# Kernel optimization log

Measured on AMD Instinct MI355X. Metric: run time of the kernel, lower is better.

Reference implementation:

```python
import jax, jax.numpy as jnp
import numpy as np

NUM_TOKENS = 1024  # codebook size (n_embed)
CODE_DIM = 256     # embedding_dim
BETA = 0.25


def setup_inputs() -> dict:
    key = jax.random.key(0)
    k1, k2 = jax.random.split(key)
    z = jax.random.normal(k1, (64, 512, CODE_DIM), dtype=jnp.float32)
    weight = jax.random.normal(k2, (NUM_TOKENS, CODE_DIM), dtype=jnp.float32)
    return {"z": z, "weight": weight}


def reference(z, weight):
    # z: [B, T, D]; weight: [K, D]
    z_flat = z.reshape(-1, CODE_DIM)                       # [N, D]
    # squared euclidean distances: ||z||^2 + ||w||^2 - 2 z.w
    d = (jnp.sum(z_flat ** 2, axis=1, keepdims=True)
         + jnp.sum(weight ** 2, axis=1)
         - 2.0 * jnp.matmul(z_flat, weight.T))             # [N, K]
    min_encoding_indices = jnp.argmin(d, axis=1)           # [N]
    z_q = weight[min_encoding_indices].reshape(z.shape)    # gather

    # perplexity from mean one-hot usage (avoid materializing one-hot via bincount)
    counts = jnp.bincount(min_encoding_indices, length=NUM_TOKENS)
    e_mean = counts.astype(z.dtype) / z_flat.shape[0]
    perplexity = jnp.exp(-jnp.sum(e_mean * jnp.log(e_mean + 1e-10)))

    # commitment loss (codebook is EMA-updated, so z_q is detached)
    loss = BETA * jnp.mean((jax.lax.stop_gradient(z_q) - z) ** 2)
    # straight-through estimator
    z_q_st = z + jax.lax.stop_gradient(z_q - z)
    return (loss, z_q_st, min_encoding_indices, perplexity)
```

## Files before the change

kernel.cpp:

```cpp
#include <hip/hip_runtime.h>

#define N_TOKENS 32768
#define K_CODES  1024
#define DIM      256
#define BETA     0.25f

typedef unsigned long long u64;
typedef _Float16 half8 __attribute__((ext_vector_type(8)));
typedef float floatx4 __attribute__((ext_vector_type(4)));

__device__ __forceinline__ int gsw(int row, int g) {
    return g ^ ((row ^ (row >> 2)) & 3);
}

__global__ void init_kernel(const float* __restrict__ w, float* __restrict__ wn,
                            int* __restrict__ counts, u64* __restrict__ keys,
                            _Float16* __restrict__ whiG, _Float16* __restrict__ wloG) {
    int k = blockIdx.x;
    int lane = threadIdx.x;
    float4 v = *(const float4*)(w + (size_t)k * DIM + lane * 4);
    float vals[4] = {v.x, v.y, v.z, v.w};
    float s = 0.f;
    #pragma unroll
    for (int e = 0; e < 4; e++) {
        s += vals[e] * vals[e];
        _Float16 h = (_Float16)vals[e];
        whiG[k * DIM + lane * 4 + e] = h;
        wloG[k * DIM + lane * 4 + e] = (_Float16)(vals[e] - (float)h);
    }
    #pragma unroll
    for (int off = 32; off; off >>= 1) s += __shfl_down(s, off);
    if (lane == 0) { wn[k] = s; counts[k] = 0; }
    if (lane < 32) keys[k * 32 + lane] = ~0ull;
}

__global__ __launch_bounds__(256, 3) void argmin_kernel(
    const float* __restrict__ z, const _Float16* __restrict__ whiG,
    const _Float16* __restrict__ wloG, const float* __restrict__ wn,
    u64* __restrict__ keys)
{
    __shared__ _Float16 zhi[128 * 32], zlo[128 * 32];
    __shared__ _Float16 whi[128 * 32], wlo[128 * 32];

    const int tid  = threadIdx.x;
    const int lane = tid & 63;
    const int wid  = tid >> 6;
    const int wm   = wid >> 1;
    const int wq   = wid & 1;
    const int t_   = blockIdx.x & 255;
    const int q    = blockIdx.x >> 8;
    const int tok0  = t_ * 128;
    const int kbase = q * 128;

    const int n  = lane & 15;
    const int kg = lane >> 4;
    const int ga = kg ^ ((n ^ (n >> 2)) & 3);

    float wnv[4];
    #pragma unroll
    for (int j = 0; j < 4; j++)
        wnv[j] = wn[kbase + wq * 64 + j * 16 + n];

    floatx4 acc[4][4];
    #pragma unroll
    for (int i = 0; i < 4; i++)
        #pragma unroll
        for (int j = 0; j < 4; j++)
            acc[i][j] = (floatx4){0.f, 0.f, 0.f, 0.f};

    const int r0 = tid >> 2;
    const int g0 = tid & 3;

    for (int dt = 0; dt < 8; ++dt) {
        const int d0 = dt * 32;
        __syncthreads();

        #pragma unroll
        for (int s = 0; s < 2; s++) {
            int t = r0 + s * 64;
            const float* p = z + (size_t)(tok0 + t) * DIM + d0 + g0 * 8;
            float4 a = *(const float4*)p;
            float4 b = *(const float4*)(p + 4);
            float vals[8] = {a.x, a.y, a.z, a.w, b.x, b.y, b.z, b.w};
            half8 hv, lv;
            #pragma unroll
            for (int e = 0; e < 8; e++) {
                _Float16 h = (_Float16)vals[e];
                hv[e] = h;
                lv[e] = (_Float16)(vals[e] - (float)h);
            }
            int off = t * 32 + gsw(t, g0) * 8;
            *(half8*)&zhi[off] = hv;
            *(half8*)&zlo[off] = lv;
        }
        #pragma unroll
        for (int s = 0; s < 2; s++) {
            int t = r0 + s * 64;
            size_t goff = (size_t)(kbase + t) * DIM + d0 + g0 * 8;
            int off = t * 32 + gsw(t, g0) * 8;
            *(half8*)&whi[off] = *(const half8*)&whiG[goff];
            *(half8*)&wlo[off] = *(const half8*)&wloG[goff];
        }
        __syncthreads();

        half8 ah[4], al[4];
        #pragma unroll
        for (int i = 0; i < 4; i++) {
            int off = (wm * 64 + i * 16 + n) * 32 + ga * 8;
            ah[i] = *(const half8*)&zhi[off];
            al[i] = *(const half8*)&zlo[off];
        }
        #pragma unroll
        for (int j = 0; j < 4; j++) {
            int off = (wq * 64 + j * 16 + n) * 32 + ga * 8;
            half8 bh = *(const half8*)&whi[off];
            half8 bl = *(const half8*)&wlo[off];
            #pragma unroll
            for (int i = 0; i < 4; i++) {
                acc[i][j] = __builtin_amdgcn_mfma_f32_16x16x32_f16(ah[i], bh, acc[i][j], 0, 0, 0);
                acc[i][j] = __builtin_amdgcn_mfma_f32_16x16x32_f16(ah[i], bl, acc[i][j], 0, 0, 0);
                acc[i][j] = __builtin_amdgcn_mfma_f32_16x16x32_f16(al[i], bh, acc[i][j], 0, 0, 0);
            }
        }
    }

    #pragma unroll
    for (int i = 0; i < 4; i++) {
        #pragma unroll
        for (int r = 0; r < 4; r++) {
            float bv = 3.4e38f; int bi = 0;
            #pragma unroll
            for (int j = 0; j < 4; j++) {
                float dist = wnv[j] - 2.0f * acc[i][j][r];
                if (dist < bv) { bv = dist; bi = kbase + wq * 64 + j * 16 + n; }
            }
            unsigned uu = __float_as_uint(bv);
            unsigned ss = (uu & 0x80000000u) ? ~uu : (uu | 0x80000000u);
            u64 key = ((u64)ss << 32) | (unsigned)bi;
            #pragma unroll
            for (int m = 1; m < 16; m <<= 1) {
                u64 o = __shfl_xor(key, m);
                if (o < key) key = o;
            }
            if (n == 0) {
                int token = tok0 + wm * 64 + i * 16 + kg * 4 + r;
                atomicMin(&keys[token], key);
            }
        }
    }
}

__global__ void gather_loss_kernel(const float* __restrict__ z,
                                   const float* __restrict__ w,
                                   const u64* __restrict__ keys,
                                   float* __restrict__ zq_out,
                                   float* __restrict__ idxf,
                                   int* __restrict__ counts,
                                   float* __restrict__ partials)
{
    __shared__ float red[4];
    int tid = threadIdx.x;
    int lane = tid & 63;
    int wid = blockIdx.x * 4 + (tid >> 6);
    u64 k4[4];
    #pragma unroll
    for (int it = 0; it < 4; it++)
        k4[it] = keys[wid + it * 8192];
    float s = 0.0f;
    #pragma unroll
    for (int it = 0; it < 4; it++) {
        int tok = wid + it * 8192;
        int k = (int)(unsigned)(k4[it] & 0xFFFFFFFFull);
        float4 wv = *(const float4*)(w + (size_t)k * DIM + lane * 4);
        float4 zv = *(const float4*)(z + (size_t)tok * DIM + lane * 4);
        *(float4*)(zq_out + (size_t)tok * DIM + lane * 4) = wv;
        float dx = wv.x - zv.x, dy = wv.y - zv.y, dz = wv.z - zv.z, dw = wv.w - zv.w;
        s += dx * dx + dy * dy + dz * dz + dw * dw;
        if (lane == 0) {
            idxf[tok] = (float)k;
            atomicAdd(&counts[k], 1);
        }
    }
    #pragma unroll
    for (int off = 32; off; off >>= 1) s += __shfl_down(s, off);
    if (lane == 0) red[tid >> 6] = s;
    __syncthreads();
    if (tid == 0)
        partials[blockIdx.x] = red[0] + red[1] + red[2] + red[3];
}

__global__ void finalize_kernel(const int* __restrict__ counts,
                                const float* __restrict__ partials,
                                float* __restrict__ loss_out,
                                float* __restrict__ ppl_out)
{
    __shared__ float redE[16], redL[16];
    int tid = threadIdx.x;
    float e = (float)counts[tid] * (1.0f / (float)N_TOKENS);
    float t = -e * logf(e + 1e-10f);
    float p = partials[tid] + partials[tid + 1024];
    #pragma unroll
    for (int off = 32; off; off >>= 1) {
        t += __shfl_down(t, off);
        p += __shfl_down(p, off);
    }
    if ((tid & 63) == 0) { redE[tid >> 6] = t; redL[tid >> 6] = p; }
    __syncthreads();
    if (tid == 0) {
        float se = 0.0f, sl = 0.0f;
        #pragma unroll
        for (int i = 0; i < 16; i++) { se += redE[i]; sl += redL[i]; }
        *ppl_out = expf(se);
        *loss_out = BETA * sl / (float)((size_t)N_TOKENS * DIM);
    }
}

extern "C" void kernel_launch(void* const* d_in, const int* in_sizes, int n_in,
                              void* d_out, int out_size, void* d_ws, size_t ws_size,
                              hipStream_t stream) {
    const float* z = (const float*)d_in[0];
    const float* w = (const float*)d_in[1];
    float* out = (float*)d_out;

    float* loss_out = out;
    float* zq_out   = out + 1;
    float* idxf     = out + 1 + (size_t)N_TOKENS * DIM;
    float* ppl_out  = out + (out_size - 1);

    float* wn       = (float*)d_ws;
    int*   counts   = (int*)d_ws + 1024;
    float* partials = (float*)d_ws + 2048;
    u64*   keys     = (u64*)((char*)d_ws + 16384);
    _Float16* whiG  = (_Float16*)((char*)d_ws + 16384 + (size_t)N_TOKENS * 8);
    _Float16* wloG  = whiG + (size_t)K_CODES * DIM;

    init_kernel<<<K_CODES, 64, 0, stream>>>(w, wn, counts, keys, whiG, wloG);
    argmin_kernel<<<8 * 256, 256, 0, stream>>>(z, whiG, wloG, wn, keys);
    gather_loss_kernel<<<2048, 256, 0, stream>>>(z, w, keys, zq_out, idxf, counts, partials);
    finalize_kernel<<<1, 1024, 0, stream>>>(counts, partials, loss_out, ppl_out);
}
```

Measured before the change: 164.1 us.

## Pre-split z into packed fp16 hi/lo tiles and fuse finalize into gather

Adds a prep kernel that converts z once into fp16 hi/lo pairs stored in the exact swizzled shared-memory tile layout, using the output buffer as scratch. The weight is packed the same way, so the argmin kernel's inner loop becomes plain contiguous 16-byte copies with no fp32 loads or conversions. Before, each z tile was reconverted by all 8 codebook-quarter blocks. The finalize kernel is also folded into the gather kernel through a last-block atomic counter, which removes one launch. The cost is an extra full pass over z plus writing and rereading the packed copy.

```diff
diff --git a/kernel.cpp b/kernel.cpp
--- a/kernel.cpp
+++ b/kernel.cpp
@@ -7,6 +7,7 @@
 
 typedef unsigned long long u64;
 typedef _Float16 half8 __attribute__((ext_vector_type(8)));
+typedef _Float16 half4 __attribute__((ext_vector_type(4)));
 typedef float floatx4 __attribute__((ext_vector_type(4)));
 
 __device__ __forceinline__ int gsw(int row, int g) {
@@ -15,29 +16,65 @@
 
 __global__ void init_kernel(const float* __restrict__ w, float* __restrict__ wn,
                             int* __restrict__ counts, u64* __restrict__ keys,
-                            _Float16* __restrict__ whiG, _Float16* __restrict__ wloG) {
+                            unsigned* __restrict__ done,
+                            _Float16* __restrict__ wPack) {
     int k = blockIdx.x;
     int lane = threadIdx.x;
     float4 v = *(const float4*)(w + (size_t)k * DIM + lane * 4);
     float vals[4] = {v.x, v.y, v.z, v.w};
     float s = 0.f;
+    half4 hv, lv;
     #pragma unroll
     for (int e = 0; e < 4; e++) {
         s += vals[e] * vals[e];
         _Float16 h = (_Float16)vals[e];
-        whiG[k * DIM + lane * 4 + e] = h;
-        wloG[k * DIM + lane * 4 + e] = (_Float16)(vals[e] - (float)h);
-    }
+        hv[e] = h;
+        lv[e] = (_Float16)(vals[e] - (float)h);
+    }
+    int e8 = k >> 7, r = k & 127;
+    int c = lane >> 3, g = (lane & 7) >> 1, eo = (lane & 1) * 4;
+    size_t base = (size_t)(e8 * 8 + c) * 8192 + r * 32 + gsw(r, g) * 8 + eo;
+    *(half4*)&wPack[base] = hv;
+    *(half4*)&wPack[base + 4096] = lv;
     #pragma unroll
     for (int off = 32; off; off >>= 1) s += __shfl_down(s, off);
     if (lane == 0) { wn[k] = s; counts[k] = 0; }
+    if (k == 0 && lane == 0) *done = 0u;
     if (lane < 32) keys[k * 32 + lane] = ~0ull;
 }
 
+__global__ void prep_z_kernel(const float* __restrict__ z,
+                              _Float16* __restrict__ zPack) {
+    int tid = threadIdx.x;
+    int t = blockIdx.x >> 2, p = blockIdx.x & 3;
+    #pragma unroll
+    for (int cc = 0; cc < 2; cc++) {
+        int c = p * 2 + cc;
+        #pragma unroll
+        for (int j = 0; j < 2; j++) {
+            int idx = j * 256 + tid;
+            int r = idx >> 2, g = idx & 3;
+            const float* src = z + (size_t)(t * 128 + r) * DIM + c * 32 + g * 8;
+            float4 a = *(const float4*)src;
+            float4 b = *(const float4*)(src + 4);
+            float vals[8] = {a.x, a.y, a.z, a.w, b.x, b.y, b.z, b.w};
+            half8 hv, lv;
+            #pragma unroll
+            for (int e = 0; e < 8; e++) {
+                _Float16 h = (_Float16)vals[e];
+                hv[e] = h;
+                lv[e] = (_Float16)(vals[e] - (float)h);
+            }
+            size_t base = (size_t)(t * 8 + c) * 8192 + r * 32 + gsw(r, g) * 8;
+            *(half8*)&zPack[base] = hv;
+            *(half8*)&zPack[base + 4096] = lv;
+        }
+    }
+}
+
 __global__ __launch_bounds__(256, 3) void argmin_kernel(
-    const float* __restrict__ z, const _Float16* __restrict__ whiG,
-    const _Float16* __restrict__ wloG, const float* __restrict__ wn,
-    u64* __restrict__ keys)
+    const _Float16* __restrict__ zPack, const _Float16* __restrict__ wPack,
+    const float* __restrict__ wn, u64* __restrict__ keys)
 {
     __shared__ _Float16 zhi[128 * 32], zlo[128 * 32];
     __shared__ _Float16 whi[128 * 32], wlo[128 * 32];
@@ -68,38 +105,19 @@
         for (int j = 0; j < 4; j++)
             acc[i][j] = (floatx4){0.f, 0.f, 0.f, 0.f};
 
-    const int r0 = tid >> 2;
-    const int g0 = tid & 3;
-
     for (int dt = 0; dt < 8; ++dt) {
-        const int d0 = dt * 32;
         __syncthreads();
-
-        #pragma unroll
-        for (int s = 0; s < 2; s++) {
-            int t = r0 + s * 64;
-            const float* p = z + (size_t)(tok0 + t) * DIM + d0 + g0 * 8;
-            float4 a = *(const float4*)p;
-            float4 b = *(const float4*)(p + 4);
-            float vals[8] = {a.x, a.y, a.z, a.w, b.x, b.y, b.z, b.w};
-            half8 hv, lv;
-            #pragma unroll
-            for (int e = 0; e < 8; e++) {
-                _Float16 h = (_Float16)vals[e];
-                hv[e] = h;
-                lv[e] = (_Float16)(vals[e] - (float)h);
-            }
-            int off = t * 32 + gsw(t, g0) * 8;
-            *(half8*)&zhi[off] = hv;
-            *(half8*)&zlo[off] = lv;
-        }
-        #pragma unroll
-        for (int s = 0; s < 2; s++) {
-            int t = r0 + s * 64;
-            size_t goff = (size_t)(kbase + t) * DIM + d0 + g0 * 8;
-            int off = t * 32 + gsw(t, g0) * 8;
-            *(half8*)&whi[off] = *(const half8*)&whiG[goff];
-            *(half8*)&wlo[off] = *(const half8*)&wloG[goff];
+        {
+            size_t zb = (size_t)(t_ * 8 + dt) * 8192;
+            size_t wb = (size_t)(q  * 8 + dt) * 8192;
+            #pragma unroll
+            for (int j = 0; j < 2; j++) {
+                int o = (j * 256 + tid) * 8;
+                *(half8*)&zhi[o] = *(const half8*)&zPack[zb + o];
+                *(half8*)&zlo[o] = *(const half8*)&zPack[zb + 4096 + o];
+                *(half8*)&whi[o] = *(const half8*)&wPack[wb + o];
+                *(half8*)&wlo[o] = *(const half8*)&wPack[wb + 4096 + o];
+            }
         }
         __syncthreads();
 
@@ -156,9 +174,13 @@
                                    float* __restrict__ zq_out,
                                    float* __restrict__ idxf,
                                    int* __restrict__ counts,
-                                   float* __restrict__ partials)
+                                   float* __restrict__ partials,
+                                   unsigned* __restrict__ done,
+                                   float* __restrict__ loss_out,
+                                   float* __restrict__ ppl_out)
 {
     __shared__ float red[4];
+    __shared__ int lastBlk;
     int tid = threadIdx.x;
     int lane = tid & 63;
     int wid = blockIdx.x * 4 + (tid >> 6);
@@ -185,33 +207,38 @@
     for (int off = 32; off; off >>= 1) s += __shfl_down(s, off);
     if (lane == 0) red[tid >> 6] = s;
     __syncthreads();
-    if (tid == 0)
+    if (tid == 0) {
         partials[blockIdx.x] = red[0] + red[1] + red[2] + red[3];
-}
-
-__global__ void finalize_kernel(const int* __restrict__ counts,
-                                const float* __restrict__ partials,
-                                float* __restrict__ loss_out,
-                                float* __restrict__ ppl_out)
-{
-    __shared__ float redE[16], redL[16];
-    int tid = threadIdx.x;
-    float e = (float)counts[tid] * (1.0f / (float)N_TOKENS);
-    float t = -e * logf(e + 1e-10f);
-    float p = partials[tid] + partials[tid + 1024];
-    #pragma unroll
-    for (int off = 32; off; off >>= 1) {
-        t += __shfl_down(t, off);
-        p += __shfl_down(p, off);
-    }
-    if ((tid & 63) == 0) { redE[tid >> 6] = t; redL[tid >> 6] = p; }
+        __threadfence();
+        unsigned old = atomicAdd(done, 1u);
+        lastBlk = (old == gridDim.x - 1) ? 1 : 0;
+    }
     __syncthreads();
-    if (tid == 0) {
-        float se = 0.0f, sl = 0.0f;
-        #pragma unroll
-        for (int i = 0; i < 16; i++) { se += redE[i]; sl += redL[i]; }
-        *ppl_out = expf(se);
-        *loss_out = BETA * sl / (float)((size_t)N_TOKENS * DIM);
+    if (lastBlk) {
+        __threadfence();
+        float t = 0.f, p = 0.f;
+        #pragma unroll
+        for (int i = 0; i < 4; i++) {
+            float e = (float)counts[tid * 4 + i] * (1.0f / (float)N_TOKENS);
+            t += -e * logf(e + 1e-10f);
+        }
+        #pragma unroll
+        for (int i = 0; i < 8; i++)
+            p += partials[tid + i * 256];
+        __shared__ float redE[4], redL[4];
+        #pragma unroll
+        for (int off = 32; off; off >>= 1) {
+            t += __shfl_down(t, off);
+            p += __shfl_down(p, off);
+        }
+        if (lane == 0) { redE[tid >> 6] = t; redL[tid >> 6] = p; }
+        __syncthreads();
+        if (tid == 0) {
+            float se = redE[0] + redE[1] + redE[2] + redE[3];
+            float sl = redL[0] + redL[1] + redL[2] + redL[3];
+            *ppl_out = expf(se);
+            *loss_out = BETA * sl / (float)((size_t)N_TOKENS * DIM);
+        }
     }
 }
 
@@ -227,15 +254,19 @@
     float* idxf     = out + 1 + (size_t)N_TOKENS * DIM;
     float* ppl_out  = out + (out_size - 1);
 
-    float* wn       = (float*)d_ws;
-    int*   counts   = (int*)d_ws + 1024;
-    float* partials = (float*)d_ws + 2048;
-    u64*   keys     = (u64*)((char*)d_ws + 16384);
-    _Float16* whiG  = (_Float16*)((char*)d_ws + 16384 + (size_t)N_TOKENS * 8);
-    _Float16* wloG  = whiG + (size_t)K_CODES * DIM;
-
-    init_kernel<<<K_CODES, 64, 0, stream>>>(w, wn, counts, keys, whiG, wloG);
-    argmin_kernel<<<8 * 256, 256, 0, stream>>>(z, whiG, wloG, wn, keys);
-    gather_loss_kernel<<<2048, 256, 0, stream>>>(z, w, keys, zq_out, idxf, counts, partials);
-    finalize_kernel<<<1, 1024, 0, stream>>>(counts, partials, loss_out, ppl_out);
-}
+    _Float16* zPack = (_Float16*)((char*)d_out + 16);
+
+    float*    wn       = (float*)d_ws;
+    int*      counts   = (int*)((char*)d_ws + 4096);
+    float*    partials = (float*)((char*)d_ws + 8192);
+    unsigned* done     = (unsigned*)((char*)d_ws + 16384);
+    u64*      keys     = (u64*)((char*)d_ws + 32768);
+    _Float16* wPack    = (_Float16*)((char*)d_ws + 294912);
+
+    init_kernel<<<K_CODES, 64, 0, stream>>>(w, wn, counts, keys, done, wPack);
+    prep_z_kernel<<<1024, 256, 0, stream>>>(z, zPack);
+    argmin_kernel<<<8 * 256, 256, 0, stream>>>(zPack, wPack, wn, keys);
+    gather_loss_kernel<<<2048, 256, 0, stream>>>(z, w, keys, zq_out, idxf,
+                                                 counts, partials, done,
+                                                 loss_out, ppl_out);
+}
```

Result: slower. 238.2 us (+45.1%).
